# Optimization experiments

Measured on AMD Instinct MI355X. Metric: run time of the kernel, lower is better.

## Reference

```python
import jax, jax.numpy as jnp
import numpy as np
import math

HEADS = 12
D_MODEL = 768
HEAD_DIM = D_MODEL // HEADS
B, S = 2, 2048


def setup_inputs() -> dict:
    key = jax.random.key(0)
    ks = jax.random.split(key, 12)
    scale = 1.0 / math.sqrt(D_MODEL)
    inp = {
        'q': jax.random.normal(ks[0], (B, S, D_MODEL), dtype=jnp.float32),
        'k': jax.random.normal(ks[1], (B, S, D_MODEL), dtype=jnp.float32),
        'v': jax.random.normal(ks[2], (B, S, D_MODEL), dtype=jnp.float32),
        # binary padding mask: 1 = masked-out key position
        'mask': jax.random.randint(ks[3], (B, 1, 1, S), 0, 2).astype(jnp.float32),
        'Wq': jax.random.normal(ks[4], (D_MODEL, D_MODEL), dtype=jnp.float32) * scale,
        'bq': jnp.zeros((D_MODEL,), dtype=jnp.float32),
        'Wk': jax.random.normal(ks[5], (D_MODEL, D_MODEL), dtype=jnp.float32) * scale,
        'bk': jnp.zeros((D_MODEL,), dtype=jnp.float32),
        'Wv': jax.random.normal(ks[6], (D_MODEL, D_MODEL), dtype=jnp.float32) * scale,
        'bv': jnp.zeros((D_MODEL,), dtype=jnp.float32),
        'Wo': jax.random.normal(ks[7], (D_MODEL, D_MODEL), dtype=jnp.float32) * scale,
        'bo': jnp.zeros((D_MODEL,), dtype=jnp.float32),
    }
    return inp


def _split_heads(x):
    b, s, _ = x.shape
    return x.reshape(b, s, HEADS, HEAD_DIM).transpose(0, 2, 1, 3)  # [b,h,s,dh]


def reference(q, k, v, mask, Wq, bq, Wk, bk, Wv, bv, Wo, bo):
    # Linear projections (torch Linear: x @ W.T + b)
    qw = _split_heads(q @ Wq.T + bq)
    kw = _split_heads(k @ Wk.T + bk)
    vw = _split_heads(v @ Wv.T + bv)
    scores = jnp.einsum('bhqd,bhkd->bhqk', qw, kw) / math.sqrt(HEAD_DIM)
    # torch code does scores += mask * (-inf): masked (mask!=0) positions -> -inf
    scores = jnp.where(mask != 0, -jnp.inf, scores)
    weights = jax.nn.softmax(scores, axis=-1)  # [b,h,sq,sk]
    ctx = jnp.einsum('bhqk,bhkd->bhqd', weights, vw)
    ctx = ctx.transpose(0, 2, 1, 3).reshape(q.shape[0], q.shape[1], D_MODEL)
    out = ctx @ Wo.T + bo
    return out, weights
```

## Files before the change

### kernel.cpp

```cpp
#include <hip/hip_runtime.h>

typedef __bf16 bf16x8 __attribute__((ext_vector_type(8)));
typedef __bf16 bf16x4 __attribute__((ext_vector_type(4)));
typedef float  f32x4  __attribute__((ext_vector_type(4)));

#define MFMA_BF16(a, b, c) __builtin_amdgcn_mfma_f32_16x16x32_bf16((a), (b), (c), 0, 0, 0)

static constexpr int BATCH  = 2;
static constexpr int HEADS  = 12;
static constexpr int SEQ    = 2048;
static constexpr int DHEAD  = 64;
static constexpr int DMODEL = 768;
static constexpr int M_ROWS = BATCH * SEQ;
static constexpr int OUT_ELEMS  = M_ROWS * DMODEL;
static constexpr int HEAD_ELEMS = BATCH * HEADS * SEQ * DHEAD;

__device__ __forceinline__ void split_bf16(float x, __bf16 &hi, __bf16 &lo) {
    __bf16 h = (__bf16)x;
    hi = h;
    lo = (__bf16)(x - (float)h);
}

__global__ __launch_bounds__(256) void qkv_proj_kernel(
    const float* __restrict__ qin, const float* __restrict__ kin, const float* __restrict__ vin,
    const float* __restrict__ Wq, const float* __restrict__ bq,
    const float* __restrict__ Wk, const float* __restrict__ bk,
    const float* __restrict__ Wv, const float* __restrict__ bv,
    __bf16* __restrict__ Qh_hi, __bf16* __restrict__ Qh_lo,
    __bf16* __restrict__ Kh_hi, __bf16* __restrict__ Kh_lo,
    __bf16* __restrict__ Vh)
{
    const int z = blockIdx.z;
    const float* X; const float* W; const float* bias;
    float scale = 1.0f;
    if (z == 0)      { X = qin; W = Wq; bias = bq; scale = 0.125f; }
    else if (z == 1) { X = kin; W = Wk; bias = bk; }
    else             { X = vin; W = Wv; bias = bv; }

    __shared__ __bf16 As_hi[128 * 40];
    __shared__ __bf16 As_lo[128 * 40];
    __shared__ __bf16 Bs_hi[128 * 40];
    __shared__ __bf16 Bs_lo[128 * 40];

    const int tid  = threadIdx.x;
    const int wid  = tid >> 6;
    const int lane = tid & 63;
    const int quad = lane >> 4;
    const int l15  = lane & 15;
    const int wm = (wid >> 1) * 64;
    const int wn = (wid & 1) * 64;
    const int mbase = blockIdx.x * 128;
    const int nbase = blockIdx.y * 128;

    const f32x4 zf = {0.f, 0.f, 0.f, 0.f};
    f32x4 acc[4][4];
    #pragma unroll
    for (int i = 0; i < 4; i++)
        #pragma unroll
        for (int j = 0; j < 4; j++) acc[i][j] = zf;

    for (int k0 = 0; k0 < DMODEL; k0 += 32) {
        #pragma unroll
        for (int i = 0; i < 4; i++) {
            int idx = i * 256 + tid;
            int r = idx >> 3;
            int c = (idx & 7) * 4;
            float4 a4 = *(const float4*)&X[(size_t)(mbase + r) * DMODEL + k0 + c];
            float4 b4 = *(const float4*)&W[(size_t)(nbase + r) * DMODEL + k0 + c];
            float af[4] = {a4.x, a4.y, a4.z, a4.w};
            float bf[4] = {b4.x, b4.y, b4.z, b4.w};
            bf16x4 ah4, al4, bh4, bl4;
            #pragma unroll
            for (int j = 0; j < 4; j++) {
                __bf16 hi, lo;
                split_bf16(af[j], hi, lo); ah4[j] = hi; al4[j] = lo;
                split_bf16(bf[j], hi, lo); bh4[j] = hi; bl4[j] = lo;
            }
            *(bf16x4*)&As_hi[r * 40 + c] = ah4;
            *(bf16x4*)&As_lo[r * 40 + c] = al4;
            *(bf16x4*)&Bs_hi[r * 40 + c] = bh4;
            *(bf16x4*)&Bs_lo[r * 40 + c] = bl4;
        }
        __syncthreads();

        bf16x8 ah[4], al[4], bh[4], bl[4];
        #pragma unroll
        for (int f = 0; f < 4; f++) {
            int ra = (wm + f * 16 + l15) * 40 + quad * 8;
            ah[f] = *(const bf16x8*)&As_hi[ra];
            al[f] = *(const bf16x8*)&As_lo[ra];
            int rb = (wn + f * 16 + l15) * 40 + quad * 8;
            bh[f] = *(const bf16x8*)&Bs_hi[rb];
            bl[f] = *(const bf16x8*)&Bs_lo[rb];
        }
        #pragma unroll
        for (int fi = 0; fi < 4; fi++)
            #pragma unroll
            for (int fj = 0; fj < 4; fj++) {
                acc[fi][fj] = MFMA_BF16(ah[fi], bh[fj], acc[fi][fj]);
                acc[fi][fj] = MFMA_BF16(ah[fi], bl[fj], acc[fi][fj]);
                acc[fi][fj] = MFMA_BF16(al[fi], bh[fj], acc[fi][fj]);
            }
        __syncthreads();
    }

    float bvals[4];
    #pragma unroll
    for (int fj = 0; fj < 4; fj++)
        bvals[fj] = bias[nbase + wn + fj * 16 + l15];

    #pragma unroll
    for (int fi = 0; fi < 4; fi++)
        #pragma unroll
        for (int fj = 0; fj < 4; fj++)
            #pragma unroll
            for (int r = 0; r < 4; r++) {
                int m = mbase + wm + fi * 16 + quad * 4 + r;
                int n = nbase + wn + fj * 16 + l15;
                float val = (acc[fi][fj][r] + bvals[fj]) * scale;
                __bf16 hi, lo;
                split_bf16(val, hi, lo);
                int bb = m >> 11;
                int s  = m & (SEQ - 1);
                int hh = n >> 6;
                int d  = n & 63;
                int bh_ = bb * HEADS + hh;
                if (z == 0) {
                    size_t idx = ((size_t)bh_ * SEQ + s) * DHEAD + d;
                    Qh_hi[idx] = hi; Qh_lo[idx] = lo;
                } else if (z == 1) {
                    size_t idx = ((size_t)bh_ * SEQ + s) * DHEAD + d;
                    Kh_hi[idx] = hi; Kh_lo[idx] = lo;
                } else {
                    size_t idx = ((size_t)bh_ * DHEAD + d) * SEQ + s;
                    Vh[idx] = hi;
                }
            }
}

__global__ __launch_bounds__(256) void attn_ctx_kernel(
    const __bf16* __restrict__ Qh_hi, const __bf16* __restrict__ Qh_lo,
    const __bf16* __restrict__ Kh_hi, const __bf16* __restrict__ Kh_lo,
    const __bf16* __restrict__ Vh,
    const float* __restrict__ mask,
    float* __restrict__ ctx,
    float* __restrict__ lsum)
{
    const int qt = blockIdx.x;
    const int h  = blockIdx.y;
    const int b  = blockIdx.z;
    const int bh = b * HEADS + h;

    const int tid  = threadIdx.x;
    const int wid  = tid >> 6;
    const int lane = tid & 63;
    const int quad = lane >> 4;
    const int l15  = lane & 15;
    const int qrow0 = qt * 64 + wid * 16;

    __shared__ __bf16 Ks_hi[64 * 72];
    __shared__ __bf16 Ks_lo[64 * 72];
    __shared__ __bf16 Vs[64 * 72];
    __shared__ __bf16 Ps[64 * 72];
    __shared__ float bias_s[SEQ];

    for (int i = tid; i < SEQ; i += 256)
        bias_s[i] = (mask[b * SEQ + i] != 0.0f) ? -1e30f : 0.0f;

    bf16x8 aqh[2], aql[2];
    #pragma unroll
    for (int ks = 0; ks < 2; ks++) {
        size_t off = ((size_t)bh * SEQ + qrow0 + l15) * DHEAD + ks * 32 + quad * 8;
        aqh[ks] = *(const bf16x8*)&Qh_hi[off];
        aql[ks] = *(const bf16x8*)&Qh_lo[off];
    }

    const f32x4 zf = {0.f, 0.f, 0.f, 0.f};
    f32x4 cacc[4];
    #pragma unroll
    for (int fj = 0; fj < 4; fj++) cacc[fj] = zf;
    float lrun[4] = {};

    for (int kt = 0; kt < SEQ / 64; kt++) {
        const int k0 = kt * 64;

        #pragma unroll
        for (int i = 0; i < 2; i++) {
            int idx = i * 256 + tid;
            int r = idx >> 3;
            int c = (idx & 7) * 8;
            size_t gk = ((size_t)bh * SEQ + k0 + r) * DHEAD + c;
            size_t gv = ((size_t)bh * DHEAD + r) * SEQ + k0 + c;
            *(bf16x8*)&Ks_hi[r * 72 + c] = *(const bf16x8*)&Kh_hi[gk];
            *(bf16x8*)&Ks_lo[r * 72 + c] = *(const bf16x8*)&Kh_lo[gk];
            *(bf16x8*)&Vs[r * 72 + c]    = *(const bf16x8*)&Vh[gv];
        }
        __syncthreads();

        f32x4 sacc[4];
        #pragma unroll
        for (int fj = 0; fj < 4; fj++) sacc[fj] = zf;

        #pragma unroll
        for (int ks = 0; ks < 2; ks++) {
            bf16x8 kh[4], kl[4];
            #pragma unroll
            for (int fj = 0; fj < 4; fj++) {
                int off = (fj * 16 + l15) * 72 + ks * 32 + quad * 8;
                kh[fj] = *(const bf16x8*)&Ks_hi[off];
                kl[fj] = *(const bf16x8*)&Ks_lo[off];
            }
            #pragma unroll
            for (int fj = 0; fj < 4; fj++) {
                sacc[fj] = MFMA_BF16(aqh[ks], kh[fj], sacc[fj]);
                sacc[fj] = MFMA_BF16(aqh[ks], kl[fj], sacc[fj]);
                sacc[fj] = MFMA_BF16(aql[ks], kh[fj], sacc[fj]);
            }
        }

        float tsum[4] = {};
        #pragma unroll
        for (int fj = 0; fj < 4; fj++) {
            float bias = bias_s[k0 + fj * 16 + l15];
            #pragma unroll
            for (int r = 0; r < 4; r++) {
                float s = sacc[fj][r] + bias;
                s = fminf(s, 80.0f);
                float p = __expf(s);
                int rl_ = quad * 4 + r;
                Ps[(wid * 16 + rl_) * 72 + fj * 16 + l15] = (__bf16)p;
                tsum[r] += p;
            }
        }
        #pragma unroll
        for (int r = 0; r < 4; r++) {
            float t = tsum[r];
            t += __shfl_xor(t, 1);
            t += __shfl_xor(t, 2);
            t += __shfl_xor(t, 4);
            t += __shfl_xor(t, 8);
            lrun[r] += t;
        }

        #pragma unroll
        for (int ks = 0; ks < 2; ks++) {
            bf16x8 ph = *(const bf16x8*)&Ps[(wid * 16 + l15) * 72 + ks * 32 + quad * 8];
            #pragma unroll
            for (int fj = 0; fj < 4; fj++) {
                bf16x8 vh = *(const bf16x8*)&Vs[(fj * 16 + l15) * 72 + ks * 32 + quad * 8];
                cacc[fj] = MFMA_BF16(ph, vh, cacc[fj]);
            }
        }
        __syncthreads();
    }

    #pragma unroll
    for (int r = 0; r < 4; r++) {
        int rl_ = quad * 4 + r;
        int row = qrow0 + rl_;
        float lv = lrun[r];
        if (l15 == 0)
            lsum[(size_t)bh * SEQ + row] = lv;
        float inv = 1.0f / lv;
        #pragma unroll
        for (int fj = 0; fj < 4; fj++)
            ctx[((size_t)b * SEQ + row) * DMODEL + h * DHEAD + fj * 16 + l15] =
                cacc[fj][r] * inv;
    }
}

__global__ __launch_bounds__(256) void attn_weights_kernel(
    const __bf16* __restrict__ Qh_hi, const __bf16* __restrict__ Qh_lo,
    const __bf16* __restrict__ Kh_hi, const __bf16* __restrict__ Kh_lo,
    const float* __restrict__ mask,
    const float* __restrict__ lsum,
    float* __restrict__ wout)
{
    const int qt = blockIdx.x;
    const int h  = blockIdx.y;
    const int b  = blockIdx.z;
    const int bh = b * HEADS + h;

    const int tid  = threadIdx.x;
    const int wid  = tid >> 6;
    const int lane = tid & 63;
    const int quad = lane >> 4;
    const int l15  = lane & 15;
    const int qrow0 = qt * 64 + wid * 16;

    __shared__ __bf16 Ks_hi[64 * 72];
    __shared__ __bf16 Ks_lo[64 * 72];
    __shared__ float bias_s[SEQ];

    for (int i = tid; i < SEQ; i += 256)
        bias_s[i] = (mask[b * SEQ + i] != 0.0f) ? -1e30f : 0.0f;

    bf16x8 aqh[2], aql[2];
    #pragma unroll
    for (int ks = 0; ks < 2; ks++) {
        size_t off = ((size_t)bh * SEQ + qrow0 + l15) * DHEAD + ks * 32 + quad * 8;
        aqh[ks] = *(const bf16x8*)&Qh_hi[off];
        aql[ks] = *(const bf16x8*)&Qh_lo[off];
    }

    float inv[4];
    #pragma unroll
    for (int r = 0; r < 4; r++)
        inv[r] = 1.0f / lsum[(size_t)bh * SEQ + qrow0 + quad * 4 + r];

    const f32x4 zf = {0.f, 0.f, 0.f, 0.f};

    for (int kt = 0; kt < SEQ / 64; kt++) {
        const int k0 = kt * 64;

        #pragma unroll
        for (int i = 0; i < 2; i++) {
            int idx = i * 256 + tid;
            int r = idx >> 3;
            int c = (idx & 7) * 8;
            size_t gk = ((size_t)bh * SEQ + k0 + r) * DHEAD + c;
            *(bf16x8*)&Ks_hi[r * 72 + c] = *(const bf16x8*)&Kh_hi[gk];
            *(bf16x8*)&Ks_lo[r * 72 + c] = *(const bf16x8*)&Kh_lo[gk];
        }
        __syncthreads();

        f32x4 sacc[4];
        #pragma unroll
        for (int fj = 0; fj < 4; fj++) sacc[fj] = zf;

        #pragma unroll
        for (int ks = 0; ks < 2; ks++) {
            bf16x8 kh[4], kl[4];
            #pragma unroll
            for (int fj = 0; fj < 4; fj++) {
                int off = (fj * 16 + l15) * 72 + ks * 32 + quad * 8;
                kh[fj] = *(const bf16x8*)&Ks_hi[off];
                kl[fj] = *(const bf16x8*)&Ks_lo[off];
            }
            #pragma unroll
            for (int fj = 0; fj < 4; fj++) {
                sacc[fj] = MFMA_BF16(aqh[ks], kh[fj], sacc[fj]);
                sacc[fj] = MFMA_BF16(aqh[ks], kl[fj], sacc[fj]);
                sacc[fj] = MFMA_BF16(aql[ks], kh[fj], sacc[fj]);
            }
        }

        #pragma unroll
        for (int fj = 0; fj < 4; fj++) {
            float bias = bias_s[k0 + fj * 16 + l15];
            #pragma unroll
            for (int r = 0; r < 4; r++) {
                float s = sacc[fj][r] + bias;
                s = fminf(s, 80.0f);
                float p = __expf(s);
                int row = qrow0 + quad * 4 + r;
                wout[((size_t)bh * SEQ + row) * SEQ + k0 + fj * 16 + l15] = p * inv[r];
            }
        }
        __syncthreads();
    }
}

__global__ __launch_bounds__(256) void out_proj_kernel(
    const float* __restrict__ X, const float* __restrict__ W, const float* __restrict__ bias,
    float* __restrict__ out)
{
    __shared__ __bf16 As_hi[128 * 40];
    __shared__ __bf16 As_lo[128 * 40];
    __shared__ __bf16 Bs_hi[128 * 40];
    __shared__ __bf16 Bs_lo[128 * 40];

    const int tid  = threadIdx.x;
    const int wid  = tid >> 6;
    const int lane = tid & 63;
    const int quad = lane >> 4;
    const int l15  = lane & 15;
    const int wm = (wid >> 1) * 64;
    const int wn = (wid & 1) * 64;
    const int mbase = blockIdx.x * 128;
    const int nbase = blockIdx.y * 128;

    const f32x4 zf = {0.f, 0.f, 0.f, 0.f};
    f32x4 acc[4][4];
    #pragma unroll
    for (int i = 0; i < 4; i++)
        #pragma unroll
        for (int j = 0; j < 4; j++) acc[i][j] = zf;

    for (int k0 = 0; k0 < DMODEL; k0 += 32) {
        #pragma unroll
        for (int i = 0; i < 4; i++) {
            int idx = i * 256 + tid;
            int r = idx >> 3;
            int c = (idx & 7) * 4;
            float4 a4 = *(const float4*)&X[(size_t)(mbase + r) * DMODEL + k0 + c];
            float4 b4 = *(const float4*)&W[(size_t)(nbase + r) * DMODEL + k0 + c];
            float af[4] = {a4.x, a4.y, a4.z, a4.w};
            float bf[4] = {b4.x, b4.y, b4.z, b4.w};
            bf16x4 ah4, al4, bh4, bl4;
            #pragma unroll
            for (int j = 0; j < 4; j++) {
                __bf16 hi, lo;
                split_bf16(af[j], hi, lo); ah4[j] = hi; al4[j] = lo;
                split_bf16(bf[j], hi, lo); bh4[j] = hi; bl4[j] = lo;
            }
            *(bf16x4*)&As_hi[r * 40 + c] = ah4;
            *(bf16x4*)&As_lo[r * 40 + c] = al4;
            *(bf16x4*)&Bs_hi[r * 40 + c] = bh4;
            *(bf16x4*)&Bs_lo[r * 40 + c] = bl4;
        }
        __syncthreads();

        bf16x8 ah[4], al[4], bh[4], bl[4];
        #pragma unroll
        for (int f = 0; f < 4; f++) {
            int ra = (wm + f * 16 + l15) * 40 + quad * 8;
            ah[f] = *(const bf16x8*)&As_hi[ra];
            al[f] = *(const bf16x8*)&As_lo[ra];
            int rb = (wn + f * 16 + l15) * 40 + quad * 8;
            bh[f] = *(const bf16x8*)&Bs_hi[rb];
            bl[f] = *(const bf16x8*)&Bs_lo[rb];
        }
        #pragma unroll
        for (int fi = 0; fi < 4; fi++)
            #pragma unroll
            for (int fj = 0; fj < 4; fj++) {
                acc[fi][fj] = MFMA_BF16(ah[fi], bh[fj], acc[fi][fj]);
                acc[fi][fj] = MFMA_BF16(ah[fi], bl[fj], acc[fi][fj]);
                acc[fi][fj] = MFMA_BF16(al[fi], bh[fj], acc[fi][fj]);
            }
        __syncthreads();
    }

    float bvals[4];
    #pragma unroll
    for (int fj = 0; fj < 4; fj++)
        bvals[fj] = bias[nbase + wn + fj * 16 + l15];

    #pragma unroll
    for (int fi = 0; fi < 4; fi++)
        #pragma unroll
        for (int fj = 0; fj < 4; fj++)
            #pragma unroll
            for (int r = 0; r < 4; r++) {
                int m = mbase + wm + fi * 16 + quad * 4 + r;
                int n = nbase + wn + fj * 16 + l15;
                out[(size_t)m * DMODEL + n] = acc[fi][fj][r] + bvals[fj];
            }
}

extern "C" void kernel_launch(void* const* d_in, const int* in_sizes, int n_in,
                              void* d_out, int out_size, void* d_ws, size_t ws_size,
                              hipStream_t stream) {
    (void)in_sizes; (void)n_in; (void)out_size; (void)ws_size;

    const float* q    = (const float*)d_in[0];
    const float* k    = (const float*)d_in[1];
    const float* v    = (const float*)d_in[2];
    const float* mask = (const float*)d_in[3];
    const float* Wq   = (const float*)d_in[4];
    const float* bq   = (const float*)d_in[5];
    const float* Wk   = (const float*)d_in[6];
    const float* bk   = (const float*)d_in[7];
    const float* Wv   = (const float*)d_in[8];
    const float* bv   = (const float*)d_in[9];
    const float* Wo   = (const float*)d_in[10];
    const float* bo   = (const float*)d_in[11];

    float* out  = (float*)d_out;
    float* wout = out + (size_t)OUT_ELEMS;

    __bf16* wsb = (__bf16*)d_ws;
    __bf16* Qh_hi = wsb;
    __bf16* Qh_lo = wsb + 1 * (size_t)HEAD_ELEMS;
    __bf16* Kh_hi = wsb + 2 * (size_t)HEAD_ELEMS;
    __bf16* Kh_lo = wsb + 3 * (size_t)HEAD_ELEMS;
    __bf16* Vh    = wsb + 4 * (size_t)HEAD_ELEMS;
    float*  ctx   = (float*)(wsb + 5 * (size_t)HEAD_ELEMS);
    float*  lsum  = ctx + (size_t)OUT_ELEMS;

    qkv_proj_kernel<<<dim3(32, 6, 3), 256, 0, stream>>>(
        q, k, v, Wq, bq, Wk, bk, Wv, bv,
        Qh_hi, Qh_lo, Kh_hi, Kh_lo, Vh);

    attn_ctx_kernel<<<dim3(32, 12, 2), 256, 0, stream>>>(
        Qh_hi, Qh_lo, Kh_hi, Kh_lo, Vh, mask, ctx, lsum);

    attn_weights_kernel<<<dim3(32, 12, 2), 256, 0, stream>>>(
        Qh_hi, Qh_lo, Kh_hi, Kh_lo, mask, lsum, wout);

    out_proj_kernel<<<dim3(32, 6, 1), 256, 0, stream>>>(ctx, Wo, bo, out);
}
```

Before: 726.3 us.

## Load K/V fragments directly from global memory, drop LDS staging and block barriers

Both attention kernels now read K (hi/lo) and V MFMA operands straight from global memory into registers instead of staging 64-row tiles through shared memory. Removing the staging also removes the per-tile __syncthreads, since only the per-warp Ps buffer remains, and that buffer is warp-private. sched_barrier fences are added around the PV stage. The aim is to cut LDS traffic and barrier stalls, relying on L1/L2 to serve the redundant K/V reads across the four warps, at the cost of more global load requests and exposed latency.

```diff
diff --git a/kernel.cpp b/kernel.cpp
--- a/kernel.cpp
+++ b/kernel.cpp
@@ -158,14 +158,16 @@
     const int l15  = lane & 15;
     const int qrow0 = qt * 64 + wid * 16;
 
-    __shared__ __bf16 Ks_hi[64 * 72];
-    __shared__ __bf16 Ks_lo[64 * 72];
-    __shared__ __bf16 Vs[64 * 72];
     __shared__ __bf16 Ps[64 * 72];
     __shared__ float bias_s[SEQ];
 
     for (int i = tid; i < SEQ; i += 256)
         bias_s[i] = (mask[b * SEQ + i] != 0.0f) ? -1e30f : 0.0f;
+    __syncthreads();
+
+    const __bf16* Kh_hi_b = Kh_hi + (size_t)bh * SEQ * DHEAD;
+    const __bf16* Kh_lo_b = Kh_lo + (size_t)bh * SEQ * DHEAD;
+    const __bf16* Vh_b    = Vh    + (size_t)bh * DHEAD * SEQ;
 
     bf16x8 aqh[2], aql[2];
     #pragma unroll
@@ -184,19 +186,6 @@
     for (int kt = 0; kt < SEQ / 64; kt++) {
         const int k0 = kt * 64;
 
-        #pragma unroll
-        for (int i = 0; i < 2; i++) {
-            int idx = i * 256 + tid;
-            int r = idx >> 3;
-            int c = (idx & 7) * 8;
-            size_t gk = ((size_t)bh * SEQ + k0 + r) * DHEAD + c;
-            size_t gv = ((size_t)bh * DHEAD + r) * SEQ + k0 + c;
-            *(bf16x8*)&Ks_hi[r * 72 + c] = *(const bf16x8*)&Kh_hi[gk];
-            *(bf16x8*)&Ks_lo[r * 72 + c] = *(const bf16x8*)&Kh_lo[gk];
-            *(bf16x8*)&Vs[r * 72 + c]    = *(const bf16x8*)&Vh[gv];
-        }
-        __syncthreads();
-
         f32x4 sacc[4];
         #pragma unroll
         for (int fj = 0; fj < 4; fj++) sacc[fj] = zf;
@@ -206,9 +195,9 @@
             bf16x8 kh[4], kl[4];
             #pragma unroll
             for (int fj = 0; fj < 4; fj++) {
-                int off = (fj * 16 + l15) * 72 + ks * 32 + quad * 8;
-                kh[fj] = *(const bf16x8*)&Ks_hi[off];
-                kl[fj] = *(const bf16x8*)&Ks_lo[off];
+                size_t off = (size_t)(k0 + fj * 16 + l15) * DHEAD + ks * 32 + quad * 8;
+                kh[fj] = *(const bf16x8*)&Kh_hi_b[off];
+                kl[fj] = *(const bf16x8*)&Kh_lo_b[off];
             }
             #pragma unroll
             for (int fj = 0; fj < 4; fj++) {
@@ -227,8 +216,7 @@
                 float s = sacc[fj][r] + bias;
                 s = fminf(s, 80.0f);
                 float p = __expf(s);
-                int rl_ = quad * 4 + r;
-                Ps[(wid * 16 + rl_) * 72 + fj * 16 + l15] = (__bf16)p;
+                Ps[(wid * 16 + quad * 4 + r) * 72 + fj * 16 + l15] = (__bf16)p;
                 tsum[r] += p;
             }
         }
@@ -242,16 +230,19 @@
             lrun[r] += t;
         }
 
+        __builtin_amdgcn_sched_barrier(0);
+
         #pragma unroll
         for (int ks = 0; ks < 2; ks++) {
             bf16x8 ph = *(const bf16x8*)&Ps[(wid * 16 + l15) * 72 + ks * 32 + quad * 8];
             #pragma unroll
             for (int fj = 0; fj < 4; fj++) {
-                bf16x8 vh = *(const bf16x8*)&Vs[(fj * 16 + l15) * 72 + ks * 32 + quad * 8];
+                size_t off = (size_t)(fj * 16 + l15) * SEQ + k0 + ks * 32 + quad * 8;
+                bf16x8 vh = *(const bf16x8*)&Vh_b[off];
                 cacc[fj] = MFMA_BF16(ph, vh, cacc[fj]);
             }
         }
-        __syncthreads();
+        __builtin_amdgcn_sched_barrier(0);
     }
 
     #pragma unroll
@@ -288,12 +279,13 @@
     const int l15  = lane & 15;
     const int qrow0 = qt * 64 + wid * 16;
 
-    __shared__ __bf16 Ks_hi[64 * 72];
-    __shared__ __bf16 Ks_lo[64 * 72];
     __shared__ float bias_s[SEQ];
-
     for (int i = tid; i < SEQ; i += 256)
         bias_s[i] = (mask[b * SEQ + i] != 0.0f) ? -1e30f : 0.0f;
+    __syncthreads();
+
+    const __bf16* Kh_hi_b = Kh_hi + (size_t)bh * SEQ * DHEAD;
+    const __bf16* Kh_lo_b = Kh_lo + (size_t)bh * SEQ * DHEAD;
 
     bf16x8 aqh[2], aql[2];
     #pragma unroll
@@ -313,17 +305,6 @@
     for (int kt = 0; kt < SEQ / 64; kt++) {
         const int k0 = kt * 64;
 
-        #pragma unroll
-        for (int i = 0; i < 2; i++) {
-            int idx = i * 256 + tid;
-            int r = idx >> 3;
-            int c = (idx & 7) * 8;
-            size_t gk = ((size_t)bh * SEQ + k0 + r) * DHEAD + c;
-            *(bf16x8*)&Ks_hi[r * 72 + c] = *(const bf16x8*)&Kh_hi[gk];
-            *(bf16x8*)&Ks_lo[r * 72 + c] = *(const bf16x8*)&Kh_lo[gk];
-        }
-        __syncthreads();
-
         f32x4 sacc[4];
         #pragma unroll
         for (int fj = 0; fj < 4; fj++) sacc[fj] = zf;
@@ -333,9 +314,9 @@
             bf16x8 kh[4], kl[4];
             #pragma unroll
             for (int fj = 0; fj < 4; fj++) {
-                int off = (fj * 16 + l15) * 72 + ks * 32 + quad * 8;
-                kh[fj] = *(const bf16x8*)&Ks_hi[off];
-                kl[fj] = *(const bf16x8*)&Ks_lo[off];
+                size_t off = (size_t)(k0 + fj * 16 + l15) * DHEAD + ks * 32 + quad * 8;
+                kh[fj] = *(const bf16x8*)&Kh_hi_b[off];
+                kl[fj] = *(const bf16x8*)&Kh_lo_b[off];
             }
             #pragma unroll
             for (int fj = 0; fj < 4; fj++) {
@@ -357,7 +338,6 @@
                 wout[((size_t)bh * SEQ + row) * SEQ + k0 + fj * 16 + l15] = p * inv[r];
             }
         }
-        __syncthreads();
     }
 }
 
```

Measured after the change: 979.7 us. 1.35x slower.
